# Optimization experiments

Measured on AMD Instinct MI355X. Metric: run time of the kernel, lower is better.

## Reference

```python
import jax, jax.numpy as jnp
import numpy as np

EPS = 1e-12  # matches torch F.normalize default eps

def _l2_normalize(x, axis):
    n = jnp.sqrt(jnp.sum(x * x, axis=axis, keepdims=True))
    return x / jnp.maximum(n, EPS)

def setup_inputs() -> dict:
    key = jax.random.key(0)
    k1, k2 = jax.random.split(key)
    feat_tar = jax.random.normal(k1, (4096, 128), dtype=jnp.float32)      # [hw, C]
    feat_refs = jax.random.normal(k2, (8, 128, 4096), dtype=jnp.float32)  # [num_ctx, C, hw]
    return {"feat_tar": feat_tar, "feat_refs": feat_refs}

def reference(feat_tar, feat_refs):
    # feature L2-normalization along channel dim (dim=1 in both tensors)
    ft = _l2_normalize(feat_tar, axis=1)    # [hw, C]
    fr = _l2_normalize(feat_refs, axis=1)   # [num_ctx, C, hw]
    # raw affinity: [num_ctx, hw_tar, hw_ref]
    affinity = jnp.einsum('tc,ncr->ntr', ft, fr)
    # affinity normalization: softmax over reference positions (last axis)
    return jax.nn.softmax(affinity, axis=-1)
```

## Files before the change

### kernel.cpp

```cpp
#include <hip/hip_runtime.h>
#include <hip/hip_bf16.h>

#define HW   4096
#define CH   128
#define NCTX 8

using bf16 = __hip_bfloat16;
typedef float f32x4 __attribute__((ext_vector_type(4)));
typedef short s16x8 __attribute__((ext_vector_type(8)));

__global__ __launch_bounds__(64) void norm_tar(const float* __restrict__ ft,
                                               bf16* __restrict__ ftn) {
    int t = blockIdx.x;
    int lane = threadIdx.x;
    float2 v = ((const float2*)(ft + (size_t)t * CH))[lane];
    float s = v.x * v.x + v.y * v.y;
    #pragma unroll
    for (int off = 1; off < 64; off <<= 1) s += __shfl_xor(s, off, 64);
    float scale = 1.0f / fmaxf(sqrtf(s), 1e-12f);
    __hip_bfloat162 h;
    h.x = __float2bfloat16(v.x * scale);
    h.y = __float2bfloat16(v.y * scale);
    ((__hip_bfloat162*)(ftn + (size_t)t * CH))[lane] = h;
}

__global__ __launch_bounds__(256) void norm_refs(const float* __restrict__ fr,
                                                 bf16* __restrict__ frt) {
    int idx = blockIdx.x * 256 + threadIdx.x;
    int n = idx >> 12;
    int r = idx & 4095;
    const float* src = fr + (size_t)n * CH * HW + r;
    float s = 0.f;
    #pragma unroll
    for (int c = 0; c < CH; ++c) {
        float v = src[(size_t)c * HW];
        s += v * v;
    }
    float scale = 1.0f / fmaxf(sqrtf(s), 1e-12f);
    bf16* dst = frt + (size_t)idx * CH;
    #pragma unroll
    for (int c0 = 0; c0 < CH; c0 += 8) {
        union { bf16 h[8]; int4 v; } u;
        #pragma unroll
        for (int j = 0; j < 8; ++j)
            u.h[j] = __float2bfloat16(src[(size_t)(c0 + j) * HW] * scale);
        ((int4*)dst)[c0 / 8] = u.v;
    }
}

template <bool WRITE>
__global__ __launch_bounds__(256) void affinity_gemm(
    const bf16* __restrict__ A, const bf16* __restrict__ Bt,
    float* __restrict__ S, float* __restrict__ out) {
    __shared__ bf16 As[128 * 128];
    __shared__ bf16 Bs[128 * 128];

    int n  = blockIdx.z;
    int t0 = blockIdx.y * 128;
    int r0 = blockIdx.x * 128;
    int tid = threadIdx.x;

    const bf16* ga = A + (size_t)t0 * CH;
    const bf16* gb = Bt + ((size_t)n * HW + r0) * CH;
    #pragma unroll
    for (int i = 0; i < 8; ++i) {
        int q = tid + i * 256;
        int row = q >> 4, c8 = q & 15;
        int4 va = ((const int4*)(ga + (size_t)row * CH))[c8];
        int4 vb = ((const int4*)(gb + (size_t)row * CH))[c8];
        int sw = c8 ^ (row & 15);
        ((int4*)As)[row * 16 + sw] = va;
        ((int4*)Bs)[row * 16 + sw] = vb;
    }
    __syncthreads();

    int wave = tid >> 6, lane = tid & 63;
    int wm = wave >> 1, wn = wave & 1;
    int l15 = lane & 15, quad = lane >> 4;

    f32x4 acc[4][4] = {};
    #pragma unroll
    for (int kc = 0; kc < 4; ++kc) {
        s16x8 af[4], bfr[4];
        #pragma unroll
        for (int i = 0; i < 4; ++i) {
            int arow = wm * 64 + i * 16 + l15;
            int brow = wn * 64 + i * 16 + l15;
            int ch = (kc * 4 + quad) ^ l15;
            af[i]  = ((const s16x8*)As)[arow * 16 + ch];
            bfr[i] = ((const s16x8*)Bs)[brow * 16 + ch];
        }
        #pragma unroll
        for (int mi = 0; mi < 4; ++mi)
            #pragma unroll
            for (int ni = 0; ni < 4; ++ni)
                acc[mi][ni] = __builtin_amdgcn_mfma_f32_16x16x32_bf16(
                    af[mi], bfr[ni], acc[mi][ni], 0, 0, 0);
    }

    if (!WRITE) {
        #pragma unroll
        for (int mi = 0; mi < 4; ++mi) {
            #pragma unroll
            for (int rg = 0; rg < 4; ++rg) {
                float rs = 0.f;
                #pragma unroll
                for (int ni = 0; ni < 4; ++ni) rs += __expf(acc[mi][ni][rg]);
                #pragma unroll
                for (int off = 1; off < 16; off <<= 1)
                    rs += __shfl_xor(rs, off, 64);
                if (l15 == 0) {
                    int row = t0 + wm * 64 + mi * 16 + quad * 4 + rg;
                    atomicAdd(&S[n * HW + row], rs);
                }
            }
        }
    } else {
        #pragma unroll
        for (int mi = 0; mi < 4; ++mi) {
            #pragma unroll
            for (int rg = 0; rg < 4; ++rg) {
                int row = t0 + wm * 64 + mi * 16 + quad * 4 + rg;
                float inv = 1.0f / S[n * HW + row];
                float* orow = out + ((size_t)n * HW + row) * HW + r0 + wn * 64;
                #pragma unroll
                for (int ni = 0; ni < 4; ++ni)
                    orow[ni * 16 + l15] = __expf(acc[mi][ni][rg]) * inv;
            }
        }
    }
}

extern "C" void kernel_launch(void* const* d_in, const int* in_sizes, int n_in,
                              void* d_out, int out_size, void* d_ws, size_t ws_size,
                              hipStream_t stream) {
    const float* ft = (const float*)d_in[0];
    const float* fr = (const float*)d_in[1];
    float* out = (float*)d_out;

    char* ws = (char*)d_ws;
    bf16* ftn = (bf16*)ws;
    bf16* frt = (bf16*)(ws + (1 << 20));
    float* S  = (float*)(ws + (9 << 20));

    hipMemsetAsync(S, 0, NCTX * HW * sizeof(float), stream);
    norm_tar<<<HW, 64, 0, stream>>>(ft, ftn);
    norm_refs<<<(NCTX * HW) / 256, 256, 0, stream>>>(fr, frt);
    affinity_gemm<false><<<dim3(32, 32, NCTX), 256, 0, stream>>>(ftn, frt, S, out);
    affinity_gemm<true ><<<dim3(32, 32, NCTX), 256, 0, stream>>>(ftn, frt, S, out);
}
```

Before: 651.9 us.

## Fuse two-pass affinity GEMM and softmax into one kernel holding full rows

Replaces the two-pass scheme, which computed the GEMM twice (once for atomic row sums, once to write), with a single kernel. Each block owns 16 target rows across all 4096 reference positions, keeps the exponentiated scores in registers, and reduces row sums through shared memory. B tiles are streamed through a double-buffered LDS pipeline, and the output uses nontemporal stores. This removes the duplicated GEMM, the atomics and the memset, at the cost of heavy register pressure (128 accumulator floats per lane), 128KB of LDS per block and low occupancy.

```diff
diff --git a/kernel.cpp b/kernel.cpp
--- a/kernel.cpp
+++ b/kernel.cpp
@@ -48,86 +48,115 @@
     }
 }
 
-template <bool WRITE>
-__global__ __launch_bounds__(256) void affinity_gemm(
-    const bf16* __restrict__ A, const bf16* __restrict__ Bt,
-    float* __restrict__ S, float* __restrict__ out) {
-    __shared__ bf16 As[128 * 128];
-    __shared__ bf16 Bs[128 * 128];
+__global__ __launch_bounds__(512) void affinity_fused(
+    const bf16* __restrict__ A,
+    const bf16* __restrict__ Bt,
+    float* __restrict__ out) {
+    __shared__ bf16 Bs[2][2][128 * 128];
+    __shared__ float Ssum[8][16];
 
-    int n  = blockIdx.z;
-    int t0 = blockIdx.y * 128;
-    int r0 = blockIdx.x * 128;
-    int tid = threadIdx.x;
+    int bid = blockIdx.x;
+    int n   = bid & 7;
+    int t0  = (bid >> 3) * 16;
 
-    const bf16* ga = A + (size_t)t0 * CH;
-    const bf16* gb = Bt + ((size_t)n * HW + r0) * CH;
+    int tid  = threadIdx.x;
+    int wave = tid >> 6, lane = tid & 63;
+    int l15  = lane & 15, quad = lane >> 4;
+
+    s16x8 af[4];
+    const s16x8* arow = (const s16x8*)(A + (size_t)(t0 + l15) * CH);
     #pragma unroll
-    for (int i = 0; i < 8; ++i) {
-        int q = tid + i * 256;
-        int row = q >> 4, c8 = q & 15;
-        int4 va = ((const int4*)(ga + (size_t)row * CH))[c8];
-        int4 vb = ((const int4*)(gb + (size_t)row * CH))[c8];
-        int sw = c8 ^ (row & 15);
-        ((int4*)As)[row * 16 + sw] = va;
-        ((int4*)Bs)[row * 16 + sw] = vb;
+    for (int kf = 0; kf < 4; ++kf) af[kf] = arow[kf * 4 + quad];
+
+    const bf16* bsrc = Bt + (size_t)n * HW * CH;
+
+    f32x4 acc[32] = {};
+    int4 stg[8];
+
+    auto GLOAD = [&](int rc) {
+        #pragma unroll
+        for (int i = 0; i < 8; ++i) {
+            int q = tid + i * 512;
+            int tile = q >> 11, q2 = q & 2047;
+            int row = q2 >> 4, c = q2 & 15;
+            stg[i] = ((const int4*)(bsrc +
+                      (size_t)(rc * 256 + tile * 128 + row) * CH))[c];
+        }
+    };
+    auto SWRITE = [&](int buf) {
+        #pragma unroll
+        for (int i = 0; i < 8; ++i) {
+            int q = tid + i * 512;
+            int tile = q >> 11, q2 = q & 2047;
+            int row = q2 >> 4, c = q2 & 15;
+            ((int4*)Bs[buf][tile])[row * 16 + (c ^ (row & 15))] = stg[i];
+        }
+    };
+
+    GLOAD(0);
+    SWRITE(0);
+    __syncthreads();
+
+    int brow = wave * 16 + l15;
+    #pragma unroll
+    for (int rc = 0; rc < 16; ++rc) {
+        int cur = rc & 1;
+        if (rc < 15) GLOAD(rc + 1);
+        #pragma unroll
+        for (int tile = 0; tile < 2; ++tile) {
+            const s16x8* bb = (const s16x8*)Bs[cur][tile];
+            s16x8 bfr[4];
+            #pragma unroll
+            for (int kf = 0; kf < 4; ++kf)
+                bfr[kf] = bb[brow * 16 + ((kf * 4 + quad) ^ l15)];
+            #pragma unroll
+            for (int kf = 0; kf < 4; ++kf)
+                acc[rc * 2 + tile] = __builtin_amdgcn_mfma_f32_16x16x32_bf16(
+                    af[kf], bfr[kf], acc[rc * 2 + tile], 0, 0, 0);
+        }
+        if (rc < 15) {
+            __syncthreads();
+            SWRITE(cur ^ 1);
+            __syncthreads();
+        }
+    }
+
+    float ps[4] = {0.f, 0.f, 0.f, 0.f};
+    #pragma unroll
+    for (int i = 0; i < 32; ++i) {
+        #pragma unroll
+        for (int rg = 0; rg < 4; ++rg) {
+            float e = __expf(acc[i][rg]);
+            acc[i][rg] = e;
+            ps[rg] += e;
+        }
+    }
+    #pragma unroll
+    for (int off = 1; off < 16; off <<= 1) {
+        #pragma unroll
+        for (int rg = 0; rg < 4; ++rg) ps[rg] += __shfl_xor(ps[rg], off, 64);
+    }
+    if (l15 == 0) {
+        #pragma unroll
+        for (int rg = 0; rg < 4; ++rg) Ssum[wave][quad * 4 + rg] = ps[rg];
     }
     __syncthreads();
-
-    int wave = tid >> 6, lane = tid & 63;
-    int wm = wave >> 1, wn = wave & 1;
-    int l15 = lane & 15, quad = lane >> 4;
-
-    f32x4 acc[4][4] = {};
+    float inv[4];
     #pragma unroll
-    for (int kc = 0; kc < 4; ++kc) {
-        s16x8 af[4], bfr[4];
+    for (int rg = 0; rg < 4; ++rg) {
+        float s = 0.f;
         #pragma unroll
-        for (int i = 0; i < 4; ++i) {
-            int arow = wm * 64 + i * 16 + l15;
-            int brow = wn * 64 + i * 16 + l15;
-            int ch = (kc * 4 + quad) ^ l15;
-            af[i]  = ((const s16x8*)As)[arow * 16 + ch];
-            bfr[i] = ((const s16x8*)Bs)[brow * 16 + ch];
-        }
+        for (int w = 0; w < 8; ++w) s += Ssum[w][quad * 4 + rg];
+        inv[rg] = 1.0f / s;
+    }
+    float* obase = out + ((size_t)n * HW + t0 + quad * 4) * HW + wave * 16 + l15;
+    #pragma unroll
+    for (int rg = 0; rg < 4; ++rg) {
+        float iv = inv[rg];
+        float* orow = obase + (size_t)rg * HW;
         #pragma unroll
-        for (int mi = 0; mi < 4; ++mi)
-            #pragma unroll
-            for (int ni = 0; ni < 4; ++ni)
-                acc[mi][ni] = __builtin_amdgcn_mfma_f32_16x16x32_bf16(
-                    af[mi], bfr[ni], acc[mi][ni], 0, 0, 0);
-    }
-
-    if (!WRITE) {
-        #pragma unroll
-        for (int mi = 0; mi < 4; ++mi) {
-            #pragma unroll
-            for (int rg = 0; rg < 4; ++rg) {
-                float rs = 0.f;
-                #pragma unroll
-                for (int ni = 0; ni < 4; ++ni) rs += __expf(acc[mi][ni][rg]);
-                #pragma unroll
-                for (int off = 1; off < 16; off <<= 1)
-                    rs += __shfl_xor(rs, off, 64);
-                if (l15 == 0) {
-                    int row = t0 + wm * 64 + mi * 16 + quad * 4 + rg;
-                    atomicAdd(&S[n * HW + row], rs);
-                }
-            }
-        }
-    } else {
-        #pragma unroll
-        for (int mi = 0; mi < 4; ++mi) {
-            #pragma unroll
-            for (int rg = 0; rg < 4; ++rg) {
-                int row = t0 + wm * 64 + mi * 16 + quad * 4 + rg;
-                float inv = 1.0f / S[n * HW + row];
-                float* orow = out + ((size_t)n * HW + row) * HW + r0 + wn * 64;
-                #pragma unroll
-                for (int ni = 0; ni < 4; ++ni)
-                    orow[ni * 16 + l15] = __expf(acc[mi][ni][rg]) * inv;
-            }
-        }
+        for (int i = 0; i < 32; ++i)
+            __builtin_nontemporal_store(acc[i][rg] * iv, orow + i * 128);
     }
 }
 
@@ -141,11 +170,8 @@
     char* ws = (char*)d_ws;
     bf16* ftn = (bf16*)ws;
     bf16* frt = (bf16*)(ws + (1 << 20));
-    float* S  = (float*)(ws + (9 << 20));
 
-    hipMemsetAsync(S, 0, NCTX * HW * sizeof(float), stream);
     norm_tar<<<HW, 64, 0, stream>>>(ft, ftn);
     norm_refs<<<(NCTX * HW) / 256, 256, 0, stream>>>(fr, frt);
-    affinity_gemm<false><<<dim3(32, 32, NCTX), 256, 0, stream>>>(ftn, frt, S, out);
-    affinity_gemm<true ><<<dim3(32, 32, NCTX), 256, 0, stream>>>(ftn, frt, S, out);
+    affinity_fused<<<NCTX * (HW / 16), 512, 0, stream>>>(ftn, frt, out);
 }
```

Result: slower. 1.135 ms (+74.0%).
